# Kernel tuning notes

Measured on AMD Instinct MI355X. Metric: run time of the kernel, lower is better.

The kernel has to match this reference:

```python
import jax, jax.numpy as jnp
import numpy as np

B, N, C = 2, 5000, 768
H, D = 12, 64
E = 160000
NEG_SLOPE = 0.2


def setup_inputs() -> dict:
    key = jax.random.key(0)
    ks = jax.random.split(key, 6)
    x = jax.random.normal(ks[0], (B, N, C), dtype=jnp.float32)
    W = jax.random.normal(ks[1], (C, H * D), dtype=jnp.float32) * 0.02
    att_src = jax.random.normal(ks[2], (H, D), dtype=jnp.float32) * 0.1
    att_dst = jax.random.normal(ks[3], (H, D), dtype=jnp.float32) * 0.1
    bias = jnp.zeros((H * D,), dtype=jnp.float32)
    edge_index = jax.random.randint(ks[4], (2, E), 0, N, dtype=jnp.int32)
    return {"x": x, "W": W, "att_src": att_src, "att_dst": att_dst,
            "bias": bias, "edge_index": edge_index}


def reference(x, W, att_src, att_dst, bias, edge_index):
    # Batched GATConv with shared edge_index (PyG defaults: self-loops,
    # leaky_relu(0.2), per-dst softmax, concat heads, bias).
    loops = jnp.arange(N, dtype=edge_index.dtype)
    src = jnp.concatenate([edge_index[0], loops])  # [Etot]
    dst = jnp.concatenate([edge_index[1], loops])

    h = (x @ W).reshape(B, N, H, D)                        # [B,N,H,D]
    a_src = jnp.einsum('bnhd,hd->bnh', h, att_src)         # [B,N,H]
    a_dst = jnp.einsum('bnhd,hd->bnh', h, att_dst)

    e = jax.nn.leaky_relu(a_src[:, src] + a_dst[:, dst], NEG_SLOPE)  # [B,Etot,H]
    e = jnp.moveaxis(e, 1, 0)                              # [Etot,B,H]

    # numerically stable softmax over edges grouped by destination node
    m = jax.ops.segment_max(e, dst, num_segments=N)        # [N,B,H]
    ex = jnp.exp(e - m[dst])
    denom = jax.ops.segment_sum(ex, dst, num_segments=N)   # [N,B,H]
    alpha = ex / (denom[dst] + 1e-16)                      # [Etot,B,H]

    h_src = jnp.moveaxis(h[:, src], 1, 0)                  # [Etot,B,H,D]
    msg = alpha[..., None] * h_src
    out = jax.ops.segment_sum(msg, dst, num_segments=N)    # [N,B,H,D]
    out = jnp.moveaxis(out, 0, 1).reshape(B, N, H * D) + bias
    return out
```

## Files before the change

kernel.cpp:

```cpp
#include <hip/hip_runtime.h>

#define Bv 2
#define Nv 5000
#define Cv 768
#define Hv 12
#define Dv 64
#define Ev 160000
#define ETOT (Ev + Nv)
#define HD 768
#define NEG 0.2f
#define Mv (Bv * Nv)
#define MPAD 10240
#define DEGMAX 128
#define DEGPAD 136
#define DEGW 132

typedef __bf16 bf16x8 __attribute__((ext_vector_type(8)));
typedef float f32x4 __attribute__((ext_vector_type(4)));

#define GLD16(gsrc, ldst)                                                      \
  __builtin_amdgcn_global_load_lds(                                            \
      (const __attribute__((address_space(1))) unsigned int*)(gsrc),           \
      (__attribute__((address_space(3))) unsigned int*)(ldst), 16, 0, 0)

__device__ __forceinline__ unsigned short f2b(float f) {
  unsigned u = __float_as_uint(f);
  return (unsigned short)((u + 0x7FFFu + ((u >> 16) & 1u)) >> 16);
}

#define NB_CVTW 576
__global__ __launch_bounds__(256) void k_pre(const float* __restrict__ W,
                                             unsigned short* __restrict__ Wt,
                                             int* __restrict__ cnt) {
  const int blk = blockIdx.x;
  const int t = threadIdx.x;
  if (blk < NB_CVTW) {
    __shared__ float s[32][33];
    const int n0 = (blk % 24) * 32, k0 = (blk / 24) * 32;
    const int tx = t & 31, ty = t >> 5;
#pragma unroll
    for (int i = 0; i < 4; ++i)
      s[ty + i * 8][tx] = W[(size_t)(k0 + ty + i * 8) * HD + n0 + tx];
    __syncthreads();
#pragma unroll
    for (int i = 0; i < 4; ++i)
      Wt[(size_t)(n0 + ty + i * 8) * Cv + k0 + tx] = f2b(s[tx][ty + i * 8]);
  } else {
    for (int i = t; i < Nv; i += 256) cnt[i] = 0;
  }
}

#define NB_GEMM 480
#define NB_SCAT ((ETOT + 255) / 256)
#define STAGEG(bi, kk)                                                         \
  {                                                                            \
    _Pragma("unroll")                                                          \
    for (int i = 0; i < 4; ++i) {                                              \
      const int r = i * 32 + rs;                                               \
      GLD16(Bt + (size_t)(bn + r) * Cv + (kk) + sl * 8, &Bs[bi][t * 8 + i * 2048]); \
    }                                                                          \
    float4 av[4][2];                                                           \
    _Pragma("unroll")                                                          \
    for (int i = 0; i < 4; ++i) {                                              \
      const int grow = bm + i * 32 + rs;                                       \
      if (grow < Mv) {                                                         \
        const float* ap = Ax + (size_t)grow * Cv + (kk) + ssl * 8;             \
        av[i][0] = *(const float4*)ap;                                         \
        av[i][1] = *(const float4*)(ap + 4);                                   \
      } else {                                                                 \
        av[i][0] = make_float4(0.f, 0.f, 0.f, 0.f);                            \
        av[i][1] = av[i][0];                                                   \
      }                                                                        \
    }                                                                          \
    _Pragma("unroll")                                                          \
    for (int i = 0; i < 4; ++i) {                                              \
      const int r = i * 32 + rs;                                               \
      unsigned short o[8];                                                     \
      o[0] = f2b(av[i][0].x); o[1] = f2b(av[i][0].y);                          \
      o[2] = f2b(av[i][0].z); o[3] = f2b(av[i][0].w);                          \
      o[4] = f2b(av[i][1].x); o[5] = f2b(av[i][1].y);                          \
      o[6] = f2b(av[i][1].z); o[7] = f2b(av[i][1].w);                          \
      const int ds = ssl ^ (r & 7);                                            \
      *(uint4*)&As[bi][r * 64 + ds * 8] = *(const uint4*)o;                    \
    }                                                                          \
  }

__global__ __launch_bounds__(256) void k_gemm_sc(const float* __restrict__ Ax,
                                                 const unsigned short* __restrict__ Bt,
                                                 unsigned short* __restrict__ C,
                                                 const float* __restrict__ att_src,
                                                 const float* __restrict__ att_dst,
                                                 float* __restrict__ asrc,
                                                 float* __restrict__ adst,
                                                 const int* __restrict__ ei,
                                                 int* __restrict__ cnt,
                                                 int* __restrict__ csrp) {
  if (blockIdx.x >= NB_GEMM) {
    const int e = (blockIdx.x - NB_GEMM) * 256 + threadIdx.x;
    if (e < ETOT) {
      int dst = (e < Ev) ? ei[Ev + e] : (e - Ev);
      int src = (e < Ev) ? ei[e] : (e - Ev);
      int pos = atomicAdd(&cnt[dst], 1);
      csrp[dst * DEGMAX + pos] = src;
    }
    return;
  }
  __shared__ unsigned short As[2][128 * 64];
  __shared__ unsigned short Bs[2][128 * 64];
  const int l0 = blockIdx.x;
  const int xcd = l0 & 7, j = l0 >> 3;
  const int bm = (xcd + 8 * (j / 6)) * 128;
  const int bn = (j % 6) * 128;
  const int t = threadIdx.x;
  const int w = t >> 6, l = t & 63;
  const int wr = w >> 1, wc = w & 1;
  const int g = l >> 4, li = l & 15;
  f32x4 acc[4][4] = {};

  const int rs = t >> 3;
  const int ssl = t & 7;
  const int sl = ssl ^ (rs & 7);

  STAGEG(0, 0);
  __syncthreads();
  int cur = 0;
#pragma unroll 1
  for (int step = 0; step < Cv / 64; ++step) {
    if (step + 1 < Cv / 64) STAGEG(cur ^ 1, (step + 1) * 64);
#pragma unroll
    for (int ks = 0; ks < 2; ++ks) {
      bf16x8 a[4], b[4];
#pragma unroll
      for (int mi = 0; mi < 4; ++mi) {
        const int row = wr * 64 + mi * 16 + li;
        const int slot = (ks * 4 + g) ^ (row & 7);
        a[mi] = *(const bf16x8*)&As[cur][row * 64 + slot * 8];
      }
#pragma unroll
      for (int nj = 0; nj < 4; ++nj) {
        const int row = wc * 64 + nj * 16 + li;
        const int slot = (ks * 4 + g) ^ (row & 7);
        b[nj] = *(const bf16x8*)&Bs[cur][row * 64 + slot * 8];
      }
#pragma unroll
      for (int mi = 0; mi < 4; ++mi)
#pragma unroll
        for (int nj = 0; nj < 4; ++nj)
          acc[mi][nj] = __builtin_amdgcn_mfma_f32_16x16x32_bf16(a[mi], b[nj], acc[mi][nj], 0, 0, 0);
    }
    __syncthreads();
    cur ^= 1;
  }
#pragma unroll
  for (int mi = 0; mi < 4; ++mi) {
#pragma unroll
    for (int nj = 0; nj < 4; ++nj) {
      const int col = bn + wc * 64 + nj * 16 + li;
#pragma unroll
      for (int r4 = 0; r4 < 4; ++r4) {
        const int row = bm + wr * 64 + mi * 16 + g * 4 + r4;
        C[(size_t)row * HD + col] = f2b(acc[mi][nj][r4]);
      }
    }
  }
  {
    const int head = (bn >> 6) + wc;
    float aS[4], aD[4];
#pragma unroll
    for (int nj = 0; nj < 4; ++nj) {
      aS[nj] = att_src[head * Dv + nj * 16 + li];
      aD[nj] = att_dst[head * Dv + nj * 16 + li];
    }
#pragma unroll
    for (int mi = 0; mi < 4; ++mi) {
#pragma unroll
      for (int r4 = 0; r4 < 4; ++r4) {
        float vs = 0.f, vd = 0.f;
#pragma unroll
        for (int nj = 0; nj < 4; ++nj) {
          const float hv = acc[mi][nj][r4];
          vs = fmaf(hv, aS[nj], vs);
          vd = fmaf(hv, aD[nj], vd);
        }
        vs += __shfl_xor(vs, 1); vd += __shfl_xor(vd, 1);
        vs += __shfl_xor(vs, 2); vd += __shfl_xor(vd, 2);
        vs += __shfl_xor(vs, 4); vd += __shfl_xor(vd, 4);
        vs += __shfl_xor(vs, 8); vd += __shfl_xor(vd, 8);
        const int row = bm + wr * 64 + mi * 16 + g * 4 + r4;
        if (li == 0 && row < Mv) {
          asrc[(size_t)row * Hv + head] = vs;
          adst[(size_t)row * Hv + head] = vd;
        }
      }
    }
  }
}

#define EDGE_FMA(c, wv)                                              \
  {                                                                  \
    acc[0] = fmaf(wv, __uint_as_float((c).x << 16), acc[0]);         \
    acc[1] = fmaf(wv, __uint_as_float((c).x & 0xFFFF0000u), acc[1]); \
    acc[2] = fmaf(wv, __uint_as_float((c).y << 16), acc[2]);         \
    acc[3] = fmaf(wv, __uint_as_float((c).y & 0xFFFF0000u), acc[3]); \
    acc[4] = fmaf(wv, __uint_as_float((c).z << 16), acc[4]);         \
    acc[5] = fmaf(wv, __uint_as_float((c).z & 0xFFFF0000u), acc[5]); \
    acc[6] = fmaf(wv, __uint_as_float((c).w << 16), acc[6]);         \
    acc[7] = fmaf(wv, __uint_as_float((c).w & 0xFFFF0000u), acc[7]); \
  }

__global__ __launch_bounds__(192) void k_agg(const unsigned short* __restrict__ h2,
                                             const int* __restrict__ cnt,
                                             const int* __restrict__ csrp,
                                             const float* __restrict__ asrc,
                                             const float* __restrict__ adst,
                                             const float* __restrict__ bias,
                                             float* __restrict__ out) {
  const int xcd = blockIdx.x & 7;
  const int idx = blockIdx.x >> 3;
  const int b = xcd >> 2;
  const int pair = (xcd & 3) * 625 + idx;
  const int n0 = pair * 2;
  const int t = threadIdx.x;
  __shared__ int s_src[2][DEGPAD];
  __shared__ float s_w[2][Hv][DEGW];
  __shared__ float s_inv[2][16];
  const int d0 = cnt[n0], d1 = cnt[n0 + 1];
  for (int i = t; i < 2 * DEGPAD; i += 192) {
    const int jn = i >= DEGPAD;
    const int ii = i - jn * DEGPAD;
    const int dd = jn ? d1 : d0;
    int sv = 0;
    if (ii < dd) sv = csrp[(n0 + jn) * DEGMAX + ii];
    s_src[jn][ii] = sv;
  }
  __syncthreads();
  {
    const int jn = t / 96, rq = t % 96;
    const int q = rq >> 5, slot = rq & 31;
    const int deg = jn ? d1 : d0;
    const int degp = (deg + 7) & ~7;
    const f32x4 adv4 = *(const f32x4*)&adst[((size_t)b * Nv + n0 + jn) * Hv + q * 4];
    f32x4 ps = {0.f, 0.f, 0.f, 0.f};
    for (int i = slot; i < deg; i += 32) {
      const int src = s_src[jn][i];
      const f32x4 as4 = *(const f32x4*)&asrc[((size_t)b * Nv + src) * Hv + q * 4];
#pragma unroll
      for (int jq = 0; jq < 4; ++jq) {
        float v = as4[jq] + adv4[jq];
        v = fmaxf(v, NEG * v);
        float ex = __expf(v);
        s_w[jn][q * 4 + jq][i] = ex;
        ps[jq] += ex;
      }
    }
    for (int i = deg + slot; i < degp; i += 32) {
#pragma unroll
      for (int jq = 0; jq < 4; ++jq) s_w[jn][q * 4 + jq][i] = 0.f;
    }
#pragma unroll
    for (int jq = 0; jq < 4; ++jq) {
      ps[jq] += __shfl_xor(ps[jq], 1);
      ps[jq] += __shfl_xor(ps[jq], 2);
      ps[jq] += __shfl_xor(ps[jq], 4);
      ps[jq] += __shfl_xor(ps[jq], 8);
      ps[jq] += __shfl_xor(ps[jq], 16);
    }
    if (slot == 0) {
      f32x4 inv;
#pragma unroll
      for (int jq = 0; jq < 4; ++jq) inv[jq] = 1.0f / (ps[jq] + 1e-16f);
      *(f32x4*)&s_inv[jn][q * 4] = inv;
    }
  }
  __syncthreads();
  const int jn = t >= 96;
  const int tl = t - jn * 96;
  const int hl = tl >> 3;
  const int degp = ((jn ? d1 : d0) + 7) & ~7;
  float acc[8] = {};
  const unsigned short* hrow = h2 + (size_t)b * Nv * HD + tl * 8;
  uint4 cA[4], cB[4];
#pragma unroll
  for (int k = 0; k < 4; ++k)
    cA[k] = *(const uint4*)(hrow + (size_t)s_src[jn][k] * HD);
  for (int base = 0; base < degp; base += 8) {
#pragma unroll
    for (int k = 0; k < 4; ++k)
      cB[k] = *(const uint4*)(hrow + (size_t)s_src[jn][base + 4 + k] * HD);
    {
      const f32x4 w4 = *(const f32x4*)&s_w[jn][hl][base];
      EDGE_FMA(cA[0], w4[0]); EDGE_FMA(cA[1], w4[1]);
      EDGE_FMA(cA[2], w4[2]); EDGE_FMA(cA[3], w4[3]);
    }
#pragma unroll
    for (int k = 0; k < 4; ++k)
      cA[k] = *(const uint4*)(hrow + (size_t)s_src[jn][base + 8 + k] * HD);
    {
      const f32x4 w4 = *(const f32x4*)&s_w[jn][hl][base + 4];
      EDGE_FMA(cB[0], w4[0]); EDGE_FMA(cB[1], w4[1]);
      EDGE_FMA(cB[2], w4[2]); EDGE_FMA(cB[3], w4[3]);
    }
  }
  const float invh = s_inv[jn][hl];
  const int od = tl * 8;
  float4 o0, o1;
  o0.x = fmaf(acc[0], invh, bias[od + 0]);
  o0.y = fmaf(acc[1], invh, bias[od + 1]);
  o0.z = fmaf(acc[2], invh, bias[od + 2]);
  o0.w = fmaf(acc[3], invh, bias[od + 3]);
  o1.x = fmaf(acc[4], invh, bias[od + 4]);
  o1.y = fmaf(acc[5], invh, bias[od + 5]);
  o1.z = fmaf(acc[6], invh, bias[od + 6]);
  o1.w = fmaf(acc[7], invh, bias[od + 7]);
  float* op = out + ((size_t)b * Nv + n0 + jn) * HD + od;
  *(float4*)op = o0;
  *(float4*)(op + 4) = o1;
}

extern "C" void kernel_launch(void* const* d_in, const int* in_sizes, int n_in,
                              void* d_out, int out_size, void* d_ws, size_t ws_size,
                              hipStream_t stream) {
  const float* x = (const float*)d_in[0];
  const float* W = (const float*)d_in[1];
  const float* att_src = (const float*)d_in[2];
  const float* att_dst = (const float*)d_in[3];
  const float* bias = (const float*)d_in[4];
  const int* ei = (const int*)d_in[5];
  float* out = (float*)d_out;

  unsigned short* h2 = (unsigned short*)d_ws;
  unsigned short* wt = h2 + (size_t)MPAD * HD;
  float* asrc = (float*)(wt + (size_t)HD * Cv);
  float* adst = asrc + (size_t)Bv * Nv * Hv;
  int* cnt = (int*)(adst + (size_t)Bv * Nv * Hv);
  int* csrp = cnt + Nv;

  k_pre<<<NB_CVTW + 1, 256, 0, stream>>>(W, wt, cnt);
  k_gemm_sc<<<NB_GEMM + NB_SCAT, 256, 0, stream>>>(x, wt, h2, att_src, att_dst,
                                                   asrc, adst, ei, cnt, csrp);
  k_agg<<<Bv * Nv / 2, 192, 0, stream>>>(h2, cnt, csrp, asrc, adst, bias, out);
}
```

Baseline: 83.56 us.

## Map each aggregation block to one node across both batches

The aggregation kernel now gives each block a single destination node and processes both batch elements with its two 96-thread halves. Before, each block handled two adjacent nodes of one batch, with an XCD-aware block swizzle. The neighbor list and degree are loaded once and shared by both batches, and both halves now run the same loop trip count, which removes divergence between halves. This gives up the XCD-based L2 locality, where each XCD's blocks touched only one batch's h2 slice, and now spreads both batches' gathers across all XCDs.

```diff
diff --git a/kernel.cpp b/kernel.cpp
--- a/kernel.cpp
+++ b/kernel.cpp
@@ -215,47 +215,39 @@
                                              const float* __restrict__ adst,
                                              const float* __restrict__ bias,
                                              float* __restrict__ out) {
-  const int xcd = blockIdx.x & 7;
-  const int idx = blockIdx.x >> 3;
-  const int b = xcd >> 2;
-  const int pair = (xcd & 3) * 625 + idx;
-  const int n0 = pair * 2;
+  const int n = blockIdx.x;
   const int t = threadIdx.x;
-  __shared__ int s_src[2][DEGPAD];
+  __shared__ int s_src[DEGPAD];
   __shared__ float s_w[2][Hv][DEGW];
   __shared__ float s_inv[2][16];
-  const int d0 = cnt[n0], d1 = cnt[n0 + 1];
-  for (int i = t; i < 2 * DEGPAD; i += 192) {
-    const int jn = i >= DEGPAD;
-    const int ii = i - jn * DEGPAD;
-    const int dd = jn ? d1 : d0;
+  const int deg = cnt[n];
+  const int degp = (deg + 7) & ~7;
+  for (int i = t; i < DEGPAD; i += 192) {
     int sv = 0;
-    if (ii < dd) sv = csrp[(n0 + jn) * DEGMAX + ii];
-    s_src[jn][ii] = sv;
+    if (i < deg) sv = csrp[n * DEGMAX + i];
+    s_src[i] = sv;
   }
   __syncthreads();
   {
-    const int jn = t / 96, rq = t % 96;
+    const int bb = t / 96, rq = t % 96;
     const int q = rq >> 5, slot = rq & 31;
-    const int deg = jn ? d1 : d0;
-    const int degp = (deg + 7) & ~7;
-    const f32x4 adv4 = *(const f32x4*)&adst[((size_t)b * Nv + n0 + jn) * Hv + q * 4];
+    const f32x4 adv4 = *(const f32x4*)&adst[((size_t)bb * Nv + n) * Hv + q * 4];
     f32x4 ps = {0.f, 0.f, 0.f, 0.f};
     for (int i = slot; i < deg; i += 32) {
-      const int src = s_src[jn][i];
-      const f32x4 as4 = *(const f32x4*)&asrc[((size_t)b * Nv + src) * Hv + q * 4];
+      const int src = s_src[i];
+      const f32x4 as4 = *(const f32x4*)&asrc[((size_t)bb * Nv + src) * Hv + q * 4];
 #pragma unroll
       for (int jq = 0; jq < 4; ++jq) {
         float v = as4[jq] + adv4[jq];
         v = fmaxf(v, NEG * v);
         float ex = __expf(v);
-        s_w[jn][q * 4 + jq][i] = ex;
+        s_w[bb][q * 4 + jq][i] = ex;
         ps[jq] += ex;
       }
     }
     for (int i = deg + slot; i < degp; i += 32) {
 #pragma unroll
-      for (int jq = 0; jq < 4; ++jq) s_w[jn][q * 4 + jq][i] = 0.f;
+      for (int jq = 0; jq < 4; ++jq) s_w[bb][q * 4 + jq][i] = 0.f;
     }
 #pragma unroll
     for (int jq = 0; jq < 4; ++jq) {
@@ -269,39 +261,38 @@
       f32x4 inv;
 #pragma unroll
       for (int jq = 0; jq < 4; ++jq) inv[jq] = 1.0f / (ps[jq] + 1e-16f);
-      *(f32x4*)&s_inv[jn][q * 4] = inv;
+      *(f32x4*)&s_inv[bb][q * 4] = inv;
     }
   }
   __syncthreads();
-  const int jn = t >= 96;
-  const int tl = t - jn * 96;
+  const int bb = t >= 96;
+  const int tl = t - bb * 96;
   const int hl = tl >> 3;
-  const int degp = ((jn ? d1 : d0) + 7) & ~7;
   float acc[8] = {};
-  const unsigned short* hrow = h2 + (size_t)b * Nv * HD + tl * 8;
+  const unsigned short* hrow = h2 + (size_t)bb * Nv * HD + tl * 8;
   uint4 cA[4], cB[4];
 #pragma unroll
   for (int k = 0; k < 4; ++k)
-    cA[k] = *(const uint4*)(hrow + (size_t)s_src[jn][k] * HD);
+    cA[k] = *(const uint4*)(hrow + (size_t)s_src[k] * HD);
   for (int base = 0; base < degp; base += 8) {
 #pragma unroll
     for (int k = 0; k < 4; ++k)
-      cB[k] = *(const uint4*)(hrow + (size_t)s_src[jn][base + 4 + k] * HD);
+      cB[k] = *(const uint4*)(hrow + (size_t)s_src[base + 4 + k] * HD);
     {
-      const f32x4 w4 = *(const f32x4*)&s_w[jn][hl][base];
+      const f32x4 w4 = *(const f32x4*)&s_w[bb][hl][base];
       EDGE_FMA(cA[0], w4[0]); EDGE_FMA(cA[1], w4[1]);
       EDGE_FMA(cA[2], w4[2]); EDGE_FMA(cA[3], w4[3]);
     }
 #pragma unroll
     for (int k = 0; k < 4; ++k)
-      cA[k] = *(const uint4*)(hrow + (size_t)s_src[jn][base + 8 + k] * HD);
+      cA[k] = *(const uint4*)(hrow + (size_t)s_src[base + 8 + k] * HD);
     {
-      const f32x4 w4 = *(const f32x4*)&s_w[jn][hl][base + 4];
+      const f32x4 w4 = *(const f32x4*)&s_w[bb][hl][base + 4];
       EDGE_FMA(cB[0], w4[0]); EDGE_FMA(cB[1], w4[1]);
       EDGE_FMA(cB[2], w4[2]); EDGE_FMA(cB[3], w4[3]);
     }
   }
-  const float invh = s_inv[jn][hl];
+  const float invh = s_inv[bb][hl];
   const int od = tl * 8;
   float4 o0, o1;
   o0.x = fmaf(acc[0], invh, bias[od + 0]);
@@ -312,7 +303,7 @@
   o1.y = fmaf(acc[5], invh, bias[od + 5]);
   o1.z = fmaf(acc[6], invh, bias[od + 6]);
   o1.w = fmaf(acc[7], invh, bias[od + 7]);
-  float* op = out + ((size_t)b * Nv + n0 + jn) * HD + od;
+  float* op = out + ((size_t)bb * Nv + n) * HD + od;
   *(float4*)op = o0;
   *(float4*)(op + 4) = o1;
 }
@@ -338,5 +329,5 @@
   k_pre<<<NB_CVTW + 1, 256, 0, stream>>>(W, wt, cnt);
   k_gemm_sc<<<NB_GEMM + NB_SCAT, 256, 0, stream>>>(x, wt, h2, att_src, att_dst,
                                                    asrc, adst, ei, cnt, csrp);
-  k_agg<<<Bv * Nv / 2, 192, 0, stream>>>(h2, cnt, csrp, asrc, adst, bias, out);
-}
+  k_agg<<<Nv, 192, 0, stream>>>(h2, cnt, csrp, asrc, adst, bias, out);
+}
```

Result: slower. 98.45 us (+17.8%).
